# Kernel optimization log

Measured on AMD Instinct MI355X. Metric: run time of the kernel, lower is better.

## Reference

```python
import jax, jax.numpy as jnp
import numpy as np

N, W, MAX_DEPTH = 250_000, 784, 16
N_NODES = 2 ** MAX_DEPTH + 1  # 65537
DEPTH = MAX_DEPTH - 1  # deepest traversal that keeps indices in-range


def setup_inputs() -> dict:
    key = jax.random.key(0)
    k1, k2, k3 = jax.random.split(key, 3)
    x = jax.random.randint(k1, (N, W), 0, 2, dtype=jnp.int32)  # binary features
    node_choices = jax.random.randint(k2, (N_NODES,), 0, W, dtype=jnp.int32)
    node_predictions = jax.random.randint(k3, (N_NODES,), 0, 2).astype(jnp.float32)
    return {"x": x, "node_choices": node_choices,
            "node_predictions": node_predictions, "depth": DEPTH}


def reference(x, node_choices, node_predictions, depth):
    # Sequential decision-tree traversal: at each level gather the split
    # feature index for every sample's current node, read that feature bit,
    # and descend to child 2*n+1 (bit=0) or 2*n+2 (bit=1).
    n = x.shape[0]
    nodes0 = jnp.zeros((n,), dtype=jnp.int32)

    def body(_, nodes):
        choices = node_choices[nodes]                                   # [n]
        decisions = jnp.take_along_axis(x, choices[:, None].astype(jnp.int32), axis=1)[:, 0]
        return nodes * 2 + decisions + 1

    nodes = jax.lax.fori_loop(0, depth, body, nodes0)
    return node_predictions[nodes].astype(jnp.bool_)
```

## Files before the change

### kernel.cpp

```cpp
#include <hip/hip_runtime.h>


#define WPR 28

__global__ __launch_bounds__(256) void fused_kernel(
    const int*   __restrict__ x,
    const int*   __restrict__ choices,
    const float* __restrict__ preds,
    const int*   __restrict__ depth_p,
    int*         __restrict__ out,
    int n)
{
    __shared__ unsigned bits[WPR * 256];

    const int tid  = threadIdx.x;
    const int lane = tid & 63;
    const int wid  = tid >> 6;
    const long long base = (long long)blockIdx.x * 256;

    for (int it = 0; it < 16; ++it) {
        const int r0 = (wid << 6) + (it << 2);

        int4 v0[4], v1[4], v2[4], v3[4];
        #pragma unroll
        for (int rr = 0; rr < 4; ++rr) {
            long long gr = base + r0 + rr;
            if (gr >= n) gr = n - 1;
            const int4* __restrict__ rowp = (const int4*)(x + gr * 784LL);
            v0[rr] = rowp[lane];
            v1[rr] = rowp[64 + lane];
            v2[rr] = rowp[128 + lane];
            v3[rr] = rowp[192 + (lane & 3)];
        }

        #pragma unroll
        for (int rr = 0; rr < 4; ++rr) {
            const int col = r0 + rr;
            unsigned long long m[12];
            #pragma unroll
            for (int cmp = 0; cmp < 4; ++cmp) {
                m[0 + cmp] = __ballot(((&v0[rr].x)[cmp] & 1) != 0);
                m[4 + cmp] = __ballot(((&v1[rr].x)[cmp] & 1) != 0);
                m[8 + cmp] = __ballot(((&v2[rr].x)[cmp] & 1) != 0);
            }
            unsigned long long t[4];
            #pragma unroll
            for (int cmp = 0; cmp < 4; ++cmp)
                t[cmp] = __ballot(((&v3[rr].x)[cmp] & 1) != 0);

            if (lane < 2) {
                #pragma unroll
                for (int q = 0; q < 12; ++q) {
                    const int w = ((q >> 2) << 3) + ((q & 3) << 1) + lane;
                    bits[w * 256 + col] = (unsigned)(m[q] >> (lane << 5));
                }
            }
            if (lane == 0) {
                #pragma unroll
                for (int cmp = 0; cmp < 4; ++cmp)
                    bits[(24 + cmp) * 256 + col] = (unsigned)t[cmp];
            }
        }
    }

    const long long i = base + tid;
    if (i >= n) return;

    const int depth = *depth_p;
    int node = 0;
    for (int d = 0; d < depth; ++d) {
        const int c  = choices[node];
        int w;
        if (c < 768) w = ((c >> 8) << 3) | ((c & 3) << 1) | ((c >> 7) & 1);
        else         w = 24 | (c & 3);
        const unsigned wv = bits[w * 256 + tid];
        node = (node << 1) + (int)((wv >> ((c >> 2) & 31)) & 1u) + 1;
    }
    out[i] = (preds[node] != 0.0f) ? 1 : 0;
}

__global__ __launch_bounds__(256) void direct_kernel(
    const int*   __restrict__ x,
    const int*   __restrict__ choices,
    const float* __restrict__ preds,
    const int*   __restrict__ depth_p,
    int*         __restrict__ out,
    int n, int w)
{
    const int i = blockIdx.x * blockDim.x + threadIdx.x;
    if (i >= n) return;
    const int depth = *depth_p;
    const int* __restrict__ row = x + (long long)i * (long long)w;
    int node = 0;
    for (int d = 0; d < depth; ++d) {
        const int c   = choices[node];
        const int bit = row[c];
        node = node * 2 + bit + 1;
    }
    out[i] = (preds[node] != 0.0f) ? 1 : 0;
}

extern "C" void kernel_launch(void* const* d_in, const int* in_sizes, int n_in,
                              void* d_out, int out_size, void* d_ws, size_t ws_size,
                              hipStream_t stream) {
    const int*   x       = (const int*)d_in[0];
    const int*   choices = (const int*)d_in[1];
    const float* preds   = (const float*)d_in[2];
    const int*   depth_p = (const int*)d_in[3];
    int*         out     = (int*)d_out;

    const int n = out_size;
    const int w = in_sizes[0] / n;

    const int block = 256;
    const int grid  = (n + block - 1) / block;

    if (w == 784) {
        fused_kernel<<<grid, block, 0, stream>>>(x, choices, preds, depth_p,
                                                 out, n);
    } else {
        direct_kernel<<<grid, block, 0, stream>>>(x, choices, preds, depth_p,
                                                  out, n, w);
    }
}
```

Before: 978.3 us.

## Software-pipeline row loads with double-buffered registers in fused bit-packing kernel

```diff
diff --git a/kernel.cpp b/kernel.cpp
--- a/kernel.cpp
+++ b/kernel.cpp
@@ -2,6 +2,42 @@
 
 
 #define WPR 28
+
+struct RowRegs { int4 p0, p1, p2, p3; };
+
+__device__ __forceinline__ void load_row(RowRegs& R, const int* __restrict__ x,
+                                         long long gr, int lane) {
+    const int4* __restrict__ rp = (const int4*)(x + gr * 784LL);
+    R.p0 = rp[lane];
+    R.p1 = rp[64 + lane];
+    R.p2 = rp[128 + lane];
+    R.p3 = rp[192 + (lane & 3)];
+}
+
+__device__ __forceinline__ void process_row(const RowRegs& R,
+                                            unsigned* __restrict__ bits,
+                                            int col, int lane) {
+    unsigned long long m[12], t[4];
+    #pragma unroll
+    for (int cmp = 0; cmp < 4; ++cmp) {
+        m[0 + cmp] = __ballot(((&R.p0.x)[cmp] & 1) != 0);
+        m[4 + cmp] = __ballot(((&R.p1.x)[cmp] & 1) != 0);
+        m[8 + cmp] = __ballot(((&R.p2.x)[cmp] & 1) != 0);
+        t[cmp]     = __ballot(((&R.p3.x)[cmp] & 1) != 0);
+    }
+    if (lane < 2) {
+        #pragma unroll
+        for (int q = 0; q < 12; ++q) {
+            const int w = ((q >> 2) << 3) + ((q & 3) << 1) + lane;
+            bits[w * 256 + col] = (unsigned)(m[q] >> (lane << 5));
+        }
+    }
+    if (lane == 0) {
+        #pragma unroll
+        for (int cmp = 0; cmp < 4; ++cmp)
+            bits[(24 + cmp) * 256 + col] = (unsigned)t[cmp];
+    }
+}
 
 __global__ __launch_bounds__(256) void fused_kernel(
     const int*   __restrict__ x,
@@ -17,50 +53,30 @@
     const int lane = tid & 63;
     const int wid  = tid >> 6;
     const long long base = (long long)blockIdx.x * 256;
+    const int wr0  = wid << 6;
 
-    for (int it = 0; it < 16; ++it) {
-        const int r0 = (wid << 6) + (it << 2);
+    auto graddr = [&](int r) -> long long {
+        const long long g = base + wr0 + r;
+        return (g < n) ? g : (long long)(n - 1);
+    };
 
-        int4 v0[4], v1[4], v2[4], v3[4];
-        #pragma unroll
-        for (int rr = 0; rr < 4; ++rr) {
-            long long gr = base + r0 + rr;
-            if (gr >= n) gr = n - 1;
-            const int4* __restrict__ rowp = (const int4*)(x + gr * 784LL);
-            v0[rr] = rowp[lane];
-            v1[rr] = rowp[64 + lane];
-            v2[rr] = rowp[128 + lane];
-            v3[rr] = rowp[192 + (lane & 3)];
+    RowRegs A0, A1, B0, B1;
+    load_row(A0, x, graddr(0), lane);
+    load_row(A1, x, graddr(1), lane);
+
+    #pragma unroll 1
+    for (int s = 0; s < 16; ++s) {
+        const int r = s << 2;
+        load_row(B0, x, graddr(r + 2), lane);
+        load_row(B1, x, graddr(r + 3), lane);
+        process_row(A0, bits, wr0 + r,     lane);
+        process_row(A1, bits, wr0 + r + 1, lane);
+        if (s < 15) {
+            load_row(A0, x, graddr(r + 4), lane);
+            load_row(A1, x, graddr(r + 5), lane);
         }
-
-        #pragma unroll
-        for (int rr = 0; rr < 4; ++rr) {
-            const int col = r0 + rr;
-            unsigned long long m[12];
-            #pragma unroll
-            for (int cmp = 0; cmp < 4; ++cmp) {
-                m[0 + cmp] = __ballot(((&v0[rr].x)[cmp] & 1) != 0);
-                m[4 + cmp] = __ballot(((&v1[rr].x)[cmp] & 1) != 0);
-                m[8 + cmp] = __ballot(((&v2[rr].x)[cmp] & 1) != 0);
-            }
-            unsigned long long t[4];
-            #pragma unroll
-            for (int cmp = 0; cmp < 4; ++cmp)
-                t[cmp] = __ballot(((&v3[rr].x)[cmp] & 1) != 0);
-
-            if (lane < 2) {
-                #pragma unroll
-                for (int q = 0; q < 12; ++q) {
-                    const int w = ((q >> 2) << 3) + ((q & 3) << 1) + lane;
-                    bits[w * 256 + col] = (unsigned)(m[q] >> (lane << 5));
-                }
-            }
-            if (lane == 0) {
-                #pragma unroll
-                for (int cmp = 0; cmp < 4; ++cmp)
-                    bits[(24 + cmp) * 256 + col] = (unsigned)t[cmp];
-            }
-        }
+        process_row(B0, bits, wr0 + r + 2, lane);
+        process_row(B1, bits, wr0 + r + 3, lane);
     }
 
     const long long i = base + tid;
@@ -69,7 +85,7 @@
     const int depth = *depth_p;
     int node = 0;
     for (int d = 0; d < depth; ++d) {
-        const int c  = choices[node];
+        const int c = choices[node];
         int w;
         if (c < 768) w = ((c >> 8) << 3) | ((c & 3) << 1) | ((c >> 7) & 1);
         else         w = 24 | (c & 3);
```

Result: no change. 979.6 us (+0.1%).
